# Kernel tuning notes

Measured on AMD Instinct MI355X. Metric: run time of the kernel, lower is better.

Reference implementation:

```python
import jax, jax.numpy as jnp
import numpy as np

TEMPERATURE = 0.05
EPS = 1e-8  # F.cosine_similarity default eps


def setup_inputs() -> dict:
    key = jax.random.key(0)
    k1, k2 = jax.random.split(key)
    N, D = 8192, 256
    return {
        "query_embeddings": jax.random.normal(k1, (N, D), dtype=jnp.float32),
        "pos_embeddings": jax.random.normal(k2, (N, D), dtype=jnp.float32),
    }


def _normalize(x):
    # matches F.cosine_similarity: x / max(||x||, eps)
    norm = jnp.sqrt(jnp.sum(x * x, axis=-1, keepdims=True))
    return x / jnp.maximum(norm, EPS)


def reference(query_embeddings, pos_embeddings):
    q = _normalize(query_embeddings)  # [N, D]
    p = _normalize(pos_embeddings)    # [N, D]
    # cosine similarity matrix via GEMM instead of (N,N,D) broadcast
    sim = jnp.einsum("nd,md->nm", q, p) / TEMPERATURE  # [N, N]
    # cross-entropy with labels = arange(N): loss_i = logsumexp(sim_i) - sim_ii
    logz = jax.nn.logsumexp(sim, axis=-1)  # [N]
    diag = jnp.diagonal(sim)               # [N]
    loss = jnp.mean(logz - diag)
    return loss
```

## Files before the change

kernel.cpp:

```cpp
#include <hip/hip_runtime.h>
#include <hip/hip_bf16.h>

#define NROWS 8192
#define DDIM  256
#define INV_TEMP 20.0f

typedef __attribute__((ext_vector_type(8))) short bf16x8;
typedef __attribute__((ext_vector_type(4))) float f32x4;

__device__ static inline void async16(const void* g, void* l) {
    __builtin_amdgcn_global_load_lds(
        (const __attribute__((address_space(1))) void*)g,
        (__attribute__((address_space(3))) void*)l, 16, 0, 0);
}

__global__ __launch_bounds__(256) void norm_diag_kernel(
    const float* __restrict__ q, const float* __restrict__ p,
    unsigned short* __restrict__ qn, unsigned short* __restrict__ pn,
    float* __restrict__ diag)
{
    const int row  = (blockIdx.x << 2) + (threadIdx.x >> 6);
    const int lane = threadIdx.x & 63;

    const float4 qv = ((const float4*)(q + (size_t)row * DDIM))[lane];
    const float4 pv = ((const float4*)(p + (size_t)row * DDIM))[lane];

    float sq = qv.x*qv.x + qv.y*qv.y + qv.z*qv.z + qv.w*qv.w;
    float sp = pv.x*pv.x + pv.y*pv.y + pv.z*pv.z + pv.w*pv.w;
    #pragma unroll
    for (int m = 1; m < 64; m <<= 1) {
        sq += __shfl_xor(sq, m);
        sp += __shfl_xor(sp, m);
    }
    const float qs = 1.0f / fmaxf(sqrtf(sq), 1e-8f);
    const float ps = 1.0f / fmaxf(sqrtf(sp), 1e-8f);

    const float qx = qv.x*qs, qy = qv.y*qs, qz = qv.z*qs, qw = qv.w*qs;
    const float px = pv.x*ps, py = pv.y*ps, pz = pv.z*ps, pw = pv.w*ps;

    float d = qx*px + qy*py + qz*pz + qw*pw;
    #pragma unroll
    for (int m = 1; m < 64; m <<= 1) d += __shfl_xor(d, m);
    if (lane == 0) diag[row] = d * INV_TEMP;

    union { unsigned short u16[4]; uint2 v; } uq, up;
    {
        __hip_bfloat16 b;
        b = __float2bfloat16(qx); uq.u16[0] = *(unsigned short*)&b;
        b = __float2bfloat16(qy); uq.u16[1] = *(unsigned short*)&b;
        b = __float2bfloat16(qz); uq.u16[2] = *(unsigned short*)&b;
        b = __float2bfloat16(qw); uq.u16[3] = *(unsigned short*)&b;
        b = __float2bfloat16(px); up.u16[0] = *(unsigned short*)&b;
        b = __float2bfloat16(py); up.u16[1] = *(unsigned short*)&b;
        b = __float2bfloat16(pz); up.u16[2] = *(unsigned short*)&b;
        b = __float2bfloat16(pw); up.u16[3] = *(unsigned short*)&b;
    }
    *(uint2*)(qn + (size_t)row * DDIM + lane * 4) = uq.v;
    *(uint2*)(pn + (size_t)row * DDIM + lane * 4) = up.v;
}

__global__ __launch_bounds__(256, 3) void simexp_kernel(
    const unsigned short* __restrict__ qn,
    const unsigned short* __restrict__ pn,
    float* __restrict__ part)
{
    __shared__ unsigned char lds[3 * 16384];

    const int tid  = threadIdx.x;
    const int lane = tid & 63;
    const int w    = tid >> 6;
    const int wr   = w >> 1;
    const int wc   = w & 1;
    const int quad = lane >> 4;
    const int l16  = lane & 15;

    const int L   = blockIdx.y * 64 + blockIdx.x;
    const int xcd = L & 7;
    const int c   = L >> 3;
    const int rowblk = xcd * 8 + (c & 7);
    const int colblk = c >> 3;
    const int rowbase = rowblk * 128;
    const int colbase = colblk * 128;

    const unsigned short* gA0 = qn + (size_t)(rowbase + (2*w  )*16 + l16) * DDIM + quad * 8;
    const unsigned short* gA1 = qn + (size_t)(rowbase + (2*w+1)*16 + l16) * DDIM + quad * 8;
    const unsigned short* gB0 = pn + (size_t)(colbase + (2*w  )*16 + l16) * DDIM + quad * 8;
    const unsigned short* gB1 = pn + (size_t)(colbase + (2*w+1)*16 + l16) * DDIM + quad * 8;

    f32x4 acc[4][4];
    #pragma unroll
    for (int i = 0; i < 4; ++i)
        #pragma unroll
        for (int j = 0; j < 4; ++j) acc[i][j] = (f32x4)0.0f;

#define STAGE(buf, ks) do {                                             \
        unsigned char* _b = lds + (buf) * 16384;                        \
        async16(gA0 + (ks) * 32, _b +        (2*w    ) * 1024);         \
        async16(gA1 + (ks) * 32, _b +        (2*w + 1) * 1024);         \
        async16(gB0 + (ks) * 32, _b + 8192 + (2*w    ) * 1024);         \
        async16(gB1 + (ks) * 32, _b + 8192 + (2*w + 1) * 1024);         \
    } while (0)

    STAGE(0, 0);
    STAGE(1, 1);
    asm volatile("s_waitcnt vmcnt(4)" ::: "memory");
    __builtin_amdgcn_s_barrier();
    asm volatile("" ::: "memory");

    #pragma unroll
    for (int ks = 0; ks < 8; ++ks) {
        if (ks < 6) STAGE((ks + 2) % 3, ks + 2);

        const unsigned char* ba = lds + (ks % 3) * 16384;
        bf16x8 af[4], bf[4];
        #pragma unroll
        for (int i = 0; i < 4; ++i)
            af[i] = *(const bf16x8*)(ba + (wr*4 + i) * 1024 + quad * 256 + l16 * 16);
        #pragma unroll
        for (int j = 0; j < 4; ++j)
            bf[j] = *(const bf16x8*)(ba + 8192 + (wc*4 + j) * 1024 + quad * 256 + l16 * 16);

        #pragma unroll
        for (int i = 0; i < 4; ++i)
            #pragma unroll
            for (int j = 0; j < 4; ++j)
                acc[i][j] = __builtin_amdgcn_mfma_f32_16x16x32_bf16(
                    af[i], bf[j], acc[i][j], 0, 0, 0);

        if (ks < 7) {
            if (ks < 6) { asm volatile("s_waitcnt vmcnt(4)" ::: "memory"); }
            else        { asm volatile("s_waitcnt vmcnt(0)" ::: "memory"); }
            __builtin_amdgcn_s_barrier();
            asm volatile("" ::: "memory");
        }
    }
#undef STAGE

    __syncthreads();
    float* red = (float*)lds;

    #pragma unroll
    for (int i = 0; i < 4; ++i)
        #pragma unroll
        for (int r = 0; r < 4; ++r) {
            float s = __expf(acc[i][0][r] * INV_TEMP)
                    + __expf(acc[i][1][r] * INV_TEMP)
                    + __expf(acc[i][2][r] * INV_TEMP)
                    + __expf(acc[i][3][r] * INV_TEMP);
            s += __shfl_xor(s, 1);
            s += __shfl_xor(s, 2);
            s += __shfl_xor(s, 4);
            s += __shfl_xor(s, 8);
            if (l16 == 0)
                red[wc * 128 + wr * 64 + i * 16 + quad * 4 + r] = s;
        }
    __syncthreads();

    if (tid < 128)
        part[(size_t)colblk * NROWS + rowbase + tid] = red[tid] + red[128 + tid];
}

__global__ __launch_bounds__(128) void rowsum_kernel(
    const float* __restrict__ part, const float* __restrict__ diag,
    float* __restrict__ loss_part)
{
    const int row = blockIdx.x * 128 + threadIdx.x;
    float s = 0.0f;
    #pragma unroll 4
    for (int cb = 0; cb < 64; ++cb)
        s += part[(size_t)cb * NROWS + row];
    float v = logf(s) - diag[row];

    #pragma unroll
    for (int m = 1; m < 64; m <<= 1) v += __shfl_xor(v, m);
    __shared__ float wsum[2];
    if ((threadIdx.x & 63) == 0) wsum[threadIdx.x >> 6] = v;
    __syncthreads();
    if (threadIdx.x == 0) loss_part[blockIdx.x] = wsum[0] + wsum[1];
}

__global__ __launch_bounds__(64) void final_kernel(
    const float* __restrict__ loss_part, float* __restrict__ out)
{
    float v = loss_part[threadIdx.x];
    #pragma unroll
    for (int m = 1; m < 64; m <<= 1) v += __shfl_xor(v, m);
    if (threadIdx.x == 0) out[0] = v * (1.0f / NROWS);
}

extern "C" void kernel_launch(void* const* d_in, const int* in_sizes, int n_in,
                              void* d_out, int out_size, void* d_ws, size_t ws_size,
                              hipStream_t stream)
{
    const float* q = (const float*)d_in[0];
    const float* p = (const float*)d_in[1];

    char* ws = (char*)d_ws;
    unsigned short* qn   = (unsigned short*)ws;
    unsigned short* pn   = (unsigned short*)(ws + (size_t)NROWS*DDIM*2);
    float* part      = (float*)(ws + 2*(size_t)NROWS*DDIM*2);
    float* diag      = part + 64 * (size_t)NROWS;
    float* loss_part = diag + NROWS;

    norm_diag_kernel<<<NROWS/4, 256, 0, stream>>>(q, p, qn, pn, diag);

    dim3 grid(64, 64);
    simexp_kernel<<<grid, 256, 0, stream>>>(qn, pn, part);

    rowsum_kernel<<<64, 128, 0, stream>>>(part, diag, loss_part);
    final_kernel<<<1, 64, 0, stream>>>(loss_part, (float*)d_out);
}
```

Baseline: 136.1 us.

## Fuse row-sum and final reduction into GEMM kernel via atomic tickets

Removes the separate rowsum and final reduction kernels. The last block to finish each row block, detected with an atomic ticket counter, computes the log-sum minus diagonal for those rows. A second ticket picks the last row block, which reduces the 64 partial losses and writes the mean. This saves two kernel launches and their gaps, at the cost of a threadfence and an atomic per block, plus a serial tail on the last-finishing blocks. Ticket counters are reset inside the normalization kernel.

```diff
diff --git a/kernel.cpp b/kernel.cpp
--- a/kernel.cpp
+++ b/kernel.cpp
@@ -17,8 +17,11 @@
 __global__ __launch_bounds__(256) void norm_diag_kernel(
     const float* __restrict__ q, const float* __restrict__ p,
     unsigned short* __restrict__ qn, unsigned short* __restrict__ pn,
-    float* __restrict__ diag)
+    float* __restrict__ diag, int* __restrict__ tickets)
 {
+    if (blockIdx.x == 0 && threadIdx.x < 66)
+        tickets[threadIdx.x] = 0;
+
     const int row  = (blockIdx.x << 2) + (threadIdx.x >> 6);
     const int lane = threadIdx.x & 63;
 
@@ -59,10 +62,14 @@
     *(uint2*)(pn + (size_t)row * DDIM + lane * 4) = up.v;
 }
 
-__global__ __launch_bounds__(256, 3) void simexp_kernel(
+__global__ __launch_bounds__(256, 3) void simexp_fused_kernel(
     const unsigned short* __restrict__ qn,
     const unsigned short* __restrict__ pn,
-    float* __restrict__ part)
+    float* __restrict__ part,
+    const float* __restrict__ diag,
+    float* __restrict__ loss_part,
+    int* __restrict__ tickets,
+    float* __restrict__ out)
 {
     __shared__ unsigned char lds[3 * 16384];
 
@@ -158,34 +165,49 @@
 
     if (tid < 128)
         part[(size_t)colblk * NROWS + rowbase + tid] = red[tid] + red[128 + tid];
-}
-
-__global__ __launch_bounds__(128) void rowsum_kernel(
-    const float* __restrict__ part, const float* __restrict__ diag,
-    float* __restrict__ loss_part)
-{
-    const int row = blockIdx.x * 128 + threadIdx.x;
-    float s = 0.0f;
-    #pragma unroll 4
-    for (int cb = 0; cb < 64; ++cb)
-        s += part[(size_t)cb * NROWS + row];
-    float v = logf(s) - diag[row];
-
-    #pragma unroll
-    for (int m = 1; m < 64; m <<= 1) v += __shfl_xor(v, m);
+
+    __threadfence();
+    __syncthreads();
+    __shared__ int swin;
+    __shared__ int sdone;
     __shared__ float wsum[2];
-    if ((threadIdx.x & 63) == 0) wsum[threadIdx.x >> 6] = v;
-    __syncthreads();
-    if (threadIdx.x == 0) loss_part[blockIdx.x] = wsum[0] + wsum[1];
-}
-
-__global__ __launch_bounds__(64) void final_kernel(
-    const float* __restrict__ loss_part, float* __restrict__ out)
-{
-    float v = loss_part[threadIdx.x];
-    #pragma unroll
-    for (int m = 1; m < 64; m <<= 1) v += __shfl_xor(v, m);
-    if (threadIdx.x == 0) out[0] = v * (1.0f / NROWS);
+    if (tid == 0)
+        swin = __hip_atomic_fetch_add(&tickets[rowblk], 1,
+                   __ATOMIC_ACQ_REL, __HIP_MEMORY_SCOPE_AGENT);
+    __syncthreads();
+    if (swin != 63) return;
+
+    float v = 0.0f;
+    if (tid < 128) {
+        const int row = rowbase + tid;
+        float s = 0.0f;
+        #pragma unroll 4
+        for (int cb = 0; cb < 64; ++cb)
+            s += __hip_atomic_load(&part[(size_t)cb * NROWS + row],
+                     __ATOMIC_RELAXED, __HIP_MEMORY_SCOPE_AGENT);
+        v = logf(s) - diag[row];
+        #pragma unroll
+        for (int m = 1; m < 64; m <<= 1) v += __shfl_xor(v, m);
+        if ((tid & 63) == 0) wsum[tid >> 6] = v;
+    }
+    __syncthreads();
+    if (tid == 0) {
+        __hip_atomic_store(&loss_part[rowblk], wsum[0] + wsum[1],
+            __ATOMIC_RELEASE, __HIP_MEMORY_SCOPE_AGENT);
+        const int d = __hip_atomic_fetch_add(&tickets[64], 1,
+                          __ATOMIC_ACQ_REL, __HIP_MEMORY_SCOPE_AGENT);
+        sdone = (d == 63);
+    }
+    __syncthreads();
+    if (!sdone) return;
+
+    if (tid < 64) {
+        float x = __hip_atomic_load(&loss_part[tid],
+                      __ATOMIC_RELAXED, __HIP_MEMORY_SCOPE_AGENT);
+        #pragma unroll
+        for (int m = 1; m < 64; m <<= 1) x += __shfl_xor(x, m);
+        if (tid == 0) out[0] = x * (1.0f / NROWS);
+    }
 }
 
 extern "C" void kernel_launch(void* const* d_in, const int* in_sizes, int n_in,
@@ -201,12 +223,11 @@
     float* part      = (float*)(ws + 2*(size_t)NROWS*DDIM*2);
     float* diag      = part + 64 * (size_t)NROWS;
     float* loss_part = diag + NROWS;
-
-    norm_diag_kernel<<<NROWS/4, 256, 0, stream>>>(q, p, qn, pn, diag);
+    int*   tickets   = (int*)(loss_part + 64);
+
+    norm_diag_kernel<<<NROWS/4, 256, 0, stream>>>(q, p, qn, pn, diag, tickets);
 
     dim3 grid(64, 64);
-    simexp_kernel<<<grid, 256, 0, stream>>>(qn, pn, part);
-
-    rowsum_kernel<<<64, 128, 0, stream>>>(part, diag, loss_part);
-    final_kernel<<<1, 64, 0, stream>>>(loss_part, (float*)d_out);
-}
+    simexp_fused_kernel<<<grid, 256, 0, stream>>>(
+        qn, pn, part, diag, loss_part, tickets, (float*)d_out);
+}
```

Measured after the change: 449.1 us. 3.3x slower.
